# Kernel tuning notes

Measured on AMD Instinct MI355X. Metric: run time of the kernel, lower is better.

The kernel has to match this reference:

```python
import jax, jax.numpy as jnp
import numpy as np

DEGREE = 8
HIDDEN = 256
IN_DIM = 3
N_LAYERS = 8  # num_hidden_layers=8 -> 1 input + 6 middle + 1 output ChebyKAN layers


def cheby_layer(x, coeff):
    """x: [P, in], coeff: [in, out, degree+1] -> [P, out].
    Computes tanh(x), Chebyshev recurrence T_0..T_d, and contracts
    sum_d T_d(x)_i * coeff[i, o, d] without materializing the full basis.
    """
    x = jnp.tanh(x)
    t_prev = jnp.ones_like(x)          # T_0
    t_cur = x                          # T_1
    out = jnp.einsum('pi,io->po', t_prev, coeff[:, :, 0])
    out = out + jnp.einsum('pi,io->po', t_cur, coeff[:, :, 1])
    for d in range(2, coeff.shape[-1]):
        t_prev, t_cur = t_cur, 2.0 * x * t_cur - t_prev
        out = out + jnp.einsum('pi,io->po', t_cur, coeff[:, :, d])
    return out


def decode(pts, ws):
    h = pts
    for w in ws:
        h = cheby_layer(h, w)
    return h


def setup_inputs() -> dict:
    key = jax.random.key(0)
    k_nm, k_m, *k_ws = jax.random.split(key, 2 + N_LAYERS)
    B, N = 4, 16384
    inp = {
        'non_mnfld_pnts': jax.random.normal(k_nm, (B, N, IN_DIM), dtype=jnp.float32),
        'mnfld_pnts': jax.random.normal(k_m, (B, N, IN_DIM), dtype=jnp.float32),
    }
    dims = [IN_DIM] + [HIDDEN] * (N_LAYERS - 1) + [1]
    for i in range(N_LAYERS):
        fan_in, fan_out = dims[i], dims[i + 1]
        std = 1.0 / (fan_in * (DEGREE + 1))
        inp[f'w{i}'] = jax.random.normal(k_ws[i], (fan_in, fan_out, DEGREE + 1), dtype=jnp.float32) * std
    return inp


def reference(non_mnfld_pnts, mnfld_pnts, w0, w1, w2, w3, w4, w5, w6, w7):
    ws = [w0, w1, w2, w3, w4, w5, w6, w7]
    B = non_mnfld_pnts.shape[0]
    mnfld_pred = decode(mnfld_pnts.reshape(-1, IN_DIM), ws).reshape(B, -1)
    nonmnfld_pred = decode(non_mnfld_pnts.reshape(-1, IN_DIM), ws).reshape(B, -1)
    return (mnfld_pred, nonmnfld_pred)
```

## Files before the change

### kernel.cpp

```cpp
#include <hip/hip_runtime.h>

typedef _Float16 f16;
typedef __attribute__((ext_vector_type(4)))  _Float16 f16x4;
typedef __attribute__((ext_vector_type(8)))  _Float16 f16x8;
typedef __attribute__((ext_vector_type(16))) float    f32x16;

#define WT_L (8*256*256)

__device__ __forceinline__ float fexp2(float x) {
#if __has_builtin(__builtin_amdgcn_exp2f)
    return __builtin_amdgcn_exp2f(x);
#else
    return exp2f(x);
#endif
}

__device__ __forceinline__ float fast_tanh(float v) {
    float a = __builtin_fabsf(v);
    float e = fexp2(a * -2.8853900817779268f);
    float r = (1.0f - e) * __builtin_amdgcn_rcpf(1.0f + e);
    return __builtin_copysignf(r, v);
}

__global__ void prep_all(const float* __restrict__ w0, const float* __restrict__ w1,
                         const float* __restrict__ w2, const float* __restrict__ w3,
                         const float* __restrict__ w4, const float* __restrict__ w5,
                         const float* __restrict__ w6, const float* __restrict__ w7,
                         f16* __restrict__ wt, float* __restrict__ biasp,
                         float* __restrict__ w0t, float* __restrict__ w7p)
{
    __shared__ float red[256];
    const int bi = blockIdx.x, t = threadIdx.x;
    if (bi < 1536) {
        const int L = bi >> 8, o = bi & 255, i = t;
        const float* w;
        switch (L) { case 0: w = w1; break; case 1: w = w2; break; case 2: w = w3; break;
                     case 3: w = w4; break; case 4: w = w5; break; default: w = w6; }
        float v[9];
#pragma unroll
        for (int d = 0; d < 9; d++) v[d] = w[(i*256 + o)*9 + d];
        const int ck = i >> 4, k = i & 15;
        const int wv4 = o >> 6, nt = (o >> 5) & 1, l31 = o & 31;
        const int lane = (k >> 3)*32 + l31, e = k & 7;
        const int base = ck*4096 + wv4*1024 + nt*512 + lane*8 + e;
#pragma unroll
        for (int d = 1; d < 9; d++)
            wt[L*WT_L + (d-1)*16*4096 + base] = (f16)v[d];
        red[i] = v[0];
        __syncthreads();
#pragma unroll
        for (int s = 128; s > 0; s >>= 1) {
            if (i < s) red[i] += red[i + s];
            __syncthreads();
        }
        if (i == 0) biasp[L*256 + o] = red[0];
    } else if (bi < 1563) {
        int id = (bi - 1536)*256 + t;
        int i = id / 2304, rem = id % 2304;
        int o = rem / 9, d = rem % 9;
        w0t[(i*9 + d)*256 + o] = w0[id];
    } else {
        int id = (bi - 1563)*256 + t;
        int ch = id / 9, d = id % 9;
        w7p[ch*12 + d] = w7[id];
    }
}

__global__ void k0(const float* __restrict__ nonm, const float* __restrict__ mnf,
                   const float* __restrict__ w0t, f16* __restrict__ xg) {
    __shared__ __align__(16) f16 sh[64*256];
    const int t = threadIdx.x, b = blockIdx.x;
    const int pt = t & 63;
    const int oh = (t >> 6) * 64;
    const int pid = b*64 + pt;
    const float* src = (pid < 65536) ? mnf : nonm;
    const int sp = (pid < 65536) ? pid : pid - 65536;
    float c0 = src[sp*3 + 0];
    float c1 = src[sp*3 + 1];
    float c2 = src[sp*3 + 2];
    float xx[3] = {fast_tanh(c0), fast_tanh(c1), fast_tanh(c2)};
    float bas[27];
#pragma unroll
    for (int i = 0; i < 3; i++) {
        float t0 = 1.0f, t1 = xx[i];
        bas[i*9+0] = t0; bas[i*9+1] = t1;
        float x2 = xx[i] + xx[i];
#pragma unroll
        for (int d = 2; d < 9; d++) {
            float t2 = x2*t1 - t0;
            bas[i*9+d] = t2; t0 = t1; t1 = t2;
        }
    }
#pragma unroll 1
    for (int q = 0; q < 16; q++) {
        int o = oh + q*4;
        float4 a = {0.f, 0.f, 0.f, 0.f};
#pragma unroll
        for (int k = 0; k < 27; k++) {
            float4 wv = *(const float4*)(w0t + k*256 + o);
            a.x = fmaf(bas[k], wv.x, a.x);
            a.y = fmaf(bas[k], wv.y, a.y);
            a.z = fmaf(bas[k], wv.z, a.z);
            a.w = fmaf(bas[k], wv.w, a.w);
        }
        f16x4 hv = {(f16)fast_tanh(a.x), (f16)fast_tanh(a.y),
                    (f16)fast_tanh(a.z), (f16)fast_tanh(a.w)};
        int unit = (o >> 3) ^ (pt & 7);
        *(f16x4*)(sh + pt*256 + unit*8 + (o & 7)) = hv;
    }
    __syncthreads();
#pragma unroll
    for (int i = 0; i < 8; i++) {
        int idx = i*256 + t;
        int p2 = idx >> 5, cu = idx & 31;
        f16x8 v = *(const f16x8*)(sh + p2*256 + ((cu ^ (p2 & 7))*8));
        *(f16x8*)(xg + (size_t)b*16384 + (size_t)idx*8) = v;
    }
}

__global__ __launch_bounds__(256, 2)
void k_mid(const f16* __restrict__ wl, const float* __restrict__ biasL,
           f16* __restrict__ xg)
{
    __shared__ __align__(16) f16 xs[128*256];

    const int t    = threadIdx.x;
    const int b    = blockIdx.x;
    const int lane = t & 63;
    const int w    = t >> 6;
    const int l31  = lane & 31;
    const int half = lane >> 5;
    const int nb   = w * 64;
    const size_t tile_off = (size_t)b * 32768;

#pragma unroll
    for (int i = 0; i < 16; i++) {
        int idx = i*256 + t;
        int pt = idx >> 5, cu = idx & 31;
        f16x8 v = *(const f16x8*)(xg + tile_off + (size_t)idx*8);
        *(f16x8*)(xs + pt*256 + ((cu ^ (pt & 7))*8)) = v;
    }
    __syncthreads();

    f32x16 acc[4][2];
    const f16x8 ones = {(f16)1.f,(f16)1.f,(f16)1.f,(f16)1.f,(f16)1.f,(f16)1.f,(f16)1.f,(f16)1.f};

    const f16* wbase = wl + w*1024 + lane*8;
    float b0 = biasL[nb + l31];
    float b1 = biasL[nb + 32 + l31];
#pragma unroll
    for (int mt = 0; mt < 4; mt++)
#pragma unroll
        for (int r = 0; r < 16; r++) { acc[mt][0][r] = b0; acc[mt][1][r] = b1; }

    f16x8 xv[4], Bb[4][2];
#pragma unroll
    for (int mt = 0; mt < 4; mt++) {
        int m = mt*32 + l31;
        int unit = half ^ (m & 7);
        xv[mt] = *(const f16x8*)(xs + m*256 + unit*8);
    }
#pragma unroll
    for (int j = 0; j < 4; j++) {
        Bb[j][0] = *(const f16x8*)(wbase + j*16*4096);
        Bb[j][1] = *(const f16x8*)(wbase + j*16*4096 + 512);
    }

    f16x8 t1[4], t0v[4];
#pragma unroll 1
    for (int ck = 0; ck < 16; ck++) {
        const int ckn = (ck < 15) ? ck + 1 : 15;
#pragma unroll
        for (int mt = 0; mt < 4; mt++) {
            t1[mt]  = xv[mt];
            t0v[mt] = ones;
        }
#pragma unroll
        for (int j = 0; j < 8; j++) {
            const int ck2 = (j < 4) ? ck : ckn;
            const int j2  = (j < 4) ? (j + 4) : (j - 4);
            const int off = (j2*16 + ck2)*4096;
            f16x8 pb0 = *(const f16x8*)(wbase + off);
            f16x8 pb1 = *(const f16x8*)(wbase + off + 512);
#pragma unroll
            for (int mt = 0; mt < 4; mt++) {
                acc[mt][0] = __builtin_amdgcn_mfma_f32_32x32x16_f16(t1[mt], Bb[j&3][0], acc[mt][0], 0, 0, 0);
                acc[mt][1] = __builtin_amdgcn_mfma_f32_32x32x16_f16(t1[mt], Bb[j&3][1], acc[mt][1], 0, 0, 0);
            }
            if (j < 7) {
#pragma unroll
                for (int mt = 0; mt < 4; mt++) {
                    f16x8 tn = xv[mt]*(t1[mt] + t1[mt]) - t0v[mt];
                    t0v[mt] = t1[mt];
                    t1[mt]  = tn;
                }
            }
            if (j == 6) {
#pragma unroll
                for (int mt = 0; mt < 4; mt++) {
                    int m = mt*32 + l31;
                    int unit = (ckn*2 + half) ^ (m & 7);
                    xv[mt] = *(const f16x8*)(xs + m*256 + unit*8);
                }
            }
            Bb[j&3][0] = pb0;
            Bb[j&3][1] = pb1;
        }
    }
    __syncthreads();

#pragma unroll
    for (int mt = 0; mt < 4; mt++) {
#pragma unroll
        for (int nt = 0; nt < 2; nt++) {
            int ch = nb + nt*32 + l31;
            int cu = ch >> 3, ce = ch & 7;
#pragma unroll
            for (int r = 0; r < 16; r++) {
                int p = mt*32 + (r & 3) + 8*(r >> 2) + 4*half;
                int unit = cu ^ (p & 7);
                xs[p*256 + unit*8 + ce] = (f16)fast_tanh(acc[mt][nt][r]);
            }
        }
    }
    __syncthreads();

#pragma unroll
    for (int i = 0; i < 16; i++) {
        int idx = i*256 + t;
        int pt = idx >> 5, cu = idx & 31;
        f16x8 v = *(const f16x8*)(xs + pt*256 + ((cu ^ (pt & 7))*8));
        *(f16x8*)(xg + tile_off + (size_t)idx*8) = v;
    }
}

__global__ void k7(const f16* __restrict__ xg, const float* __restrict__ w7p,
                   float* __restrict__ out) {
    __shared__ __align__(16) f16 sh[128*256];
    const int t = threadIdx.x, b = blockIdx.x;
    const size_t tile_off = (size_t)b * 32768;
#pragma unroll
    for (int i = 0; i < 16; i++) {
        int idx = i*256 + t;
        int pt = idx >> 5, cu = idx & 31;
        f16x8 v = *(const f16x8*)(xg + tile_off + (size_t)idx*8);
        *(f16x8*)(sh + pt*256 + ((cu ^ (pt & 7))*8)) = v;
    }
    __syncthreads();

    const int pt = t & 127;
    const int seg = t >> 7;
    float s = 0.0f;
#pragma unroll 1
    for (int q = 0; q < 16; q++) {
        int u = seg*16 + q;
        int unit = u ^ (pt & 7);
        f16x8 xv = *(const f16x8*)(sh + pt*256 + unit*8);
#pragma unroll
        for (int e = 0; e < 8; e++) {
            int ch = u*8 + e;
            const float* wr = w7p + ch*12;
            float x = (float)xv[e];
            float4 wa = *(const float4*)(wr);
            float4 wb = *(const float4*)(wr + 4);
            float wc = wr[8];
            float x2 = x + x;
            float t0 = 1.0f, t1v = x;
            s = fmaf(wa.x, t0, s);
            s = fmaf(wa.y, t1v, s);
            float t2 = x2*t1v - t0;  s = fmaf(wa.z, t2, s);
            float t3 = x2*t2 - t1v;  s = fmaf(wa.w, t3, s);
            float t4 = x2*t3 - t2;   s = fmaf(wb.x, t4, s);
            float t5 = x2*t4 - t3;   s = fmaf(wb.y, t5, s);
            float t6 = x2*t5 - t4;   s = fmaf(wb.z, t6, s);
            float t7 = x2*t6 - t5;   s = fmaf(wb.w, t7, s);
            float t8 = x2*t7 - t6;   s = fmaf(wc,  t8, s);
        }
    }
    __syncthreads();
    float* red = (float*)sh;
    red[seg*128 + pt] = s;
    __syncthreads();
    if (t < 128) out[b*128 + t] = red[t] + red[128 + t];
}

extern "C" void kernel_launch(void* const* d_in, const int* in_sizes, int n_in,
                              void* d_out, int out_size, void* d_ws, size_t ws_size,
                              hipStream_t stream) {
    const float* nonm = (const float*)d_in[0];
    const float* mnf  = (const float*)d_in[1];

    char* ws = (char*)d_ws;
    f16*   wtp   = (f16*)ws;
    float* biasp = (float*)(ws + 6*WT_L*2);
    float* w0tp  = (float*)(ws + 6*WT_L*2 + 6144);
    float* w7pp  = (float*)(ws + 6*WT_L*2 + 6144 + 27648);
    f16*   xg    = (f16*)(ws + 6*WT_L*2 + 6144 + 27648 + 12288);

    prep_all<<<1572, 256, 0, stream>>>((const float*)d_in[2], (const float*)d_in[3],
                                       (const float*)d_in[4], (const float*)d_in[5],
                                       (const float*)d_in[6], (const float*)d_in[7],
                                       (const float*)d_in[8], (const float*)d_in[9],
                                       wtp, biasp, w0tp, w7pp);

    k0<<<2048, 256, 0, stream>>>(nonm, mnf, w0tp, xg);
    for (int L = 0; L < 6; L++)
        k_mid<<<1024, 256, 0, stream>>>(wtp + L*WT_L, biasp + L*256, xg);
    k7<<<1024, 256, 0, stream>>>(xg, w7pp, (float*)d_out);
}
```

Measured before the change: 1.071 ms.

## Fuse input layer and last layer into adjacent MFMA layer kernels

Folds the first Chebyshev layer (tanh, basis and 27-term FMA) into the first MFMA hidden-layer kernel, and the final scalar output layer into the last MFMA kernel, so two global activation round trips and two launches go away. The shared GEMM body is factored into a device function. It also precomputes 2x once per chunk and moves the next-chunk LDS load of x to the start of the chunk rather than inside the inner loop. In exchange the fused kernels carry more per-block work, and the layer-0 prologue now processes 128 points per block with two threads per point.

```diff
diff --git a/kernel.cpp b/kernel.cpp
--- a/kernel.cpp
+++ b/kernel.cpp
@@ -66,81 +66,16 @@
     }
 }
 
-__global__ void k0(const float* __restrict__ nonm, const float* __restrict__ mnf,
-                   const float* __restrict__ w0t, f16* __restrict__ xg) {
-    __shared__ __align__(16) f16 sh[64*256];
-    const int t = threadIdx.x, b = blockIdx.x;
-    const int pt = t & 63;
-    const int oh = (t >> 6) * 64;
-    const int pid = b*64 + pt;
-    const float* src = (pid < 65536) ? mnf : nonm;
-    const int sp = (pid < 65536) ? pid : pid - 65536;
-    float c0 = src[sp*3 + 0];
-    float c1 = src[sp*3 + 1];
-    float c2 = src[sp*3 + 2];
-    float xx[3] = {fast_tanh(c0), fast_tanh(c1), fast_tanh(c2)};
-    float bas[27];
-#pragma unroll
-    for (int i = 0; i < 3; i++) {
-        float t0 = 1.0f, t1 = xx[i];
-        bas[i*9+0] = t0; bas[i*9+1] = t1;
-        float x2 = xx[i] + xx[i];
-#pragma unroll
-        for (int d = 2; d < 9; d++) {
-            float t2 = x2*t1 - t0;
-            bas[i*9+d] = t2; t0 = t1; t1 = t2;
-        }
-    }
-#pragma unroll 1
-    for (int q = 0; q < 16; q++) {
-        int o = oh + q*4;
-        float4 a = {0.f, 0.f, 0.f, 0.f};
-#pragma unroll
-        for (int k = 0; k < 27; k++) {
-            float4 wv = *(const float4*)(w0t + k*256 + o);
-            a.x = fmaf(bas[k], wv.x, a.x);
-            a.y = fmaf(bas[k], wv.y, a.y);
-            a.z = fmaf(bas[k], wv.z, a.z);
-            a.w = fmaf(bas[k], wv.w, a.w);
-        }
-        f16x4 hv = {(f16)fast_tanh(a.x), (f16)fast_tanh(a.y),
-                    (f16)fast_tanh(a.z), (f16)fast_tanh(a.w)};
-        int unit = (o >> 3) ^ (pt & 7);
-        *(f16x4*)(sh + pt*256 + unit*8 + (o & 7)) = hv;
-    }
-    __syncthreads();
-#pragma unroll
-    for (int i = 0; i < 8; i++) {
-        int idx = i*256 + t;
-        int p2 = idx >> 5, cu = idx & 31;
-        f16x8 v = *(const f16x8*)(sh + p2*256 + ((cu ^ (p2 & 7))*8));
-        *(f16x8*)(xg + (size_t)b*16384 + (size_t)idx*8) = v;
-    }
-}
-
-__global__ __launch_bounds__(256, 2)
-void k_mid(const f16* __restrict__ wl, const float* __restrict__ biasL,
-           f16* __restrict__ xg)
-{
-    __shared__ __align__(16) f16 xs[128*256];
-
-    const int t    = threadIdx.x;
-    const int b    = blockIdx.x;
+__device__ __forceinline__ void gemm_layer(f16* __restrict__ xs,
+                                           const f16* __restrict__ wl,
+                                           const float* __restrict__ biasL,
+                                           int t)
+{
     const int lane = t & 63;
     const int w    = t >> 6;
     const int l31  = lane & 31;
     const int half = lane >> 5;
     const int nb   = w * 64;
-    const size_t tile_off = (size_t)b * 32768;
-
-#pragma unroll
-    for (int i = 0; i < 16; i++) {
-        int idx = i*256 + t;
-        int pt = idx >> 5, cu = idx & 31;
-        f16x8 v = *(const f16x8*)(xg + tile_off + (size_t)idx*8);
-        *(f16x8*)(xs + pt*256 + ((cu ^ (pt & 7))*8)) = v;
-    }
-    __syncthreads();
 
     f32x16 acc[4][2];
     const f16x8 ones = {(f16)1.f,(f16)1.f,(f16)1.f,(f16)1.f,(f16)1.f,(f16)1.f,(f16)1.f,(f16)1.f};
@@ -166,14 +101,21 @@
         Bb[j][1] = *(const f16x8*)(wbase + j*16*4096 + 512);
     }
 
-    f16x8 t1[4], t0v[4];
+    f16x8 x2[4], t1[4], t0v[4];
 #pragma unroll 1
     for (int ck = 0; ck < 16; ck++) {
         const int ckn = (ck < 15) ? ck + 1 : 15;
 #pragma unroll
         for (int mt = 0; mt < 4; mt++) {
             t1[mt]  = xv[mt];
+            x2[mt]  = xv[mt] + xv[mt];
             t0v[mt] = ones;
+        }
+#pragma unroll
+        for (int mt = 0; mt < 4; mt++) {
+            int m = mt*32 + l31;
+            int unit = (ckn*2 + half) ^ (m & 7);
+            xv[mt] = *(const f16x8*)(xs + m*256 + unit*8);
         }
 #pragma unroll
         for (int j = 0; j < 8; j++) {
@@ -190,17 +132,9 @@
             if (j < 7) {
 #pragma unroll
                 for (int mt = 0; mt < 4; mt++) {
-                    f16x8 tn = xv[mt]*(t1[mt] + t1[mt]) - t0v[mt];
+                    f16x8 tn = x2[mt]*t1[mt] - t0v[mt];
                     t0v[mt] = t1[mt];
                     t1[mt]  = tn;
-                }
-            }
-            if (j == 6) {
-#pragma unroll
-                for (int mt = 0; mt < 4; mt++) {
-                    int m = mt*32 + l31;
-                    int unit = (ckn*2 + half) ^ (m & 7);
-                    xv[mt] = *(const f16x8*)(xs + m*256 + unit*8);
                 }
             }
             Bb[j&3][0] = pb0;
@@ -224,7 +158,61 @@
         }
     }
     __syncthreads();
-
+}
+
+__global__ __launch_bounds__(256, 2)
+void kA(const float* __restrict__ nonm, const float* __restrict__ mnf,
+        const float* __restrict__ w0t, const f16* __restrict__ wt,
+        const float* __restrict__ biasL, f16* __restrict__ xg)
+{
+    __shared__ __align__(16) f16 xs[128*256];
+    const int t = threadIdx.x, b = blockIdx.x;
+
+    {
+        const int pt = t >> 1;
+        const int oh = (t & 1) * 128;
+        const int pid = b*128 + pt;
+        const float* src = (pid < 65536) ? mnf : nonm;
+        const int sp = (pid < 65536) ? pid : pid - 65536;
+        float c0 = src[sp*3 + 0];
+        float c1 = src[sp*3 + 1];
+        float c2 = src[sp*3 + 2];
+        float xx[3] = {fast_tanh(c0), fast_tanh(c1), fast_tanh(c2)};
+        float bas[27];
+#pragma unroll
+        for (int i = 0; i < 3; i++) {
+            float t0 = 1.0f, t1 = xx[i];
+            bas[i*9+0] = t0; bas[i*9+1] = t1;
+            float x2 = xx[i] + xx[i];
+#pragma unroll
+            for (int d = 2; d < 9; d++) {
+                float t2 = x2*t1 - t0;
+                bas[i*9+d] = t2; t0 = t1; t1 = t2;
+            }
+        }
+#pragma unroll 1
+        for (int q = 0; q < 32; q++) {
+            int o = oh + q*4;
+            float4 a = {0.f, 0.f, 0.f, 0.f};
+#pragma unroll
+            for (int k = 0; k < 27; k++) {
+                float4 wv = *(const float4*)(w0t + k*256 + o);
+                a.x = fmaf(bas[k], wv.x, a.x);
+                a.y = fmaf(bas[k], wv.y, a.y);
+                a.z = fmaf(bas[k], wv.z, a.z);
+                a.w = fmaf(bas[k], wv.w, a.w);
+            }
+            f16x4 hv = {(f16)fast_tanh(a.x), (f16)fast_tanh(a.y),
+                        (f16)fast_tanh(a.z), (f16)fast_tanh(a.w)};
+            int unit = (o >> 3) ^ (pt & 7);
+            *(f16x4*)(xs + pt*256 + unit*8 + (o & 7)) = hv;
+        }
+    }
+    __syncthreads();
+
+    gemm_layer(xs, wt, biasL, t);
+
+    const size_t tile_off = (size_t)b * 32768;
 #pragma unroll
     for (int i = 0; i < 16; i++) {
         int idx = i*256 + t;
@@ -234,54 +222,90 @@
     }
 }
 
-__global__ void k7(const f16* __restrict__ xg, const float* __restrict__ w7p,
-                   float* __restrict__ out) {
-    __shared__ __align__(16) f16 sh[128*256];
+__global__ __launch_bounds__(256, 2)
+void k_mid(const f16* __restrict__ wl, const float* __restrict__ biasL,
+           f16* __restrict__ xg)
+{
+    __shared__ __align__(16) f16 xs[128*256];
     const int t = threadIdx.x, b = blockIdx.x;
     const size_t tile_off = (size_t)b * 32768;
+
 #pragma unroll
     for (int i = 0; i < 16; i++) {
         int idx = i*256 + t;
         int pt = idx >> 5, cu = idx & 31;
         f16x8 v = *(const f16x8*)(xg + tile_off + (size_t)idx*8);
-        *(f16x8*)(sh + pt*256 + ((cu ^ (pt & 7))*8)) = v;
-    }
-    __syncthreads();
-
-    const int pt = t & 127;
-    const int seg = t >> 7;
-    float s = 0.0f;
+        *(f16x8*)(xs + pt*256 + ((cu ^ (pt & 7))*8)) = v;
+    }
+    __syncthreads();
+
+    gemm_layer(xs, wl, biasL, t);
+
+#pragma unroll
+    for (int i = 0; i < 16; i++) {
+        int idx = i*256 + t;
+        int pt = idx >> 5, cu = idx & 31;
+        f16x8 v = *(const f16x8*)(xs + pt*256 + ((cu ^ (pt & 7))*8));
+        *(f16x8*)(xg + tile_off + (size_t)idx*8) = v;
+    }
+}
+
+__global__ __launch_bounds__(256, 2)
+void kC(const f16* __restrict__ wt, const float* __restrict__ biasL,
+        const float* __restrict__ w7p, const f16* __restrict__ xg,
+        float* __restrict__ out)
+{
+    __shared__ __align__(16) f16 xs[128*256];
+    const int t = threadIdx.x, b = blockIdx.x;
+    const size_t tile_off = (size_t)b * 32768;
+
+#pragma unroll
+    for (int i = 0; i < 16; i++) {
+        int idx = i*256 + t;
+        int pt = idx >> 5, cu = idx & 31;
+        f16x8 v = *(const f16x8*)(xg + tile_off + (size_t)idx*8);
+        *(f16x8*)(xs + pt*256 + ((cu ^ (pt & 7))*8)) = v;
+    }
+    __syncthreads();
+
+    gemm_layer(xs, wt, biasL, t);
+
+    {
+        const int pt = t & 127;
+        const int seg = t >> 7;
+        float s = 0.0f;
 #pragma unroll 1
-    for (int q = 0; q < 16; q++) {
-        int u = seg*16 + q;
-        int unit = u ^ (pt & 7);
-        f16x8 xv = *(const f16x8*)(sh + pt*256 + unit*8);
-#pragma unroll
-        for (int e = 0; e < 8; e++) {
-            int ch = u*8 + e;
-            const float* wr = w7p + ch*12;
-            float x = (float)xv[e];
-            float4 wa = *(const float4*)(wr);
-            float4 wb = *(const float4*)(wr + 4);
-            float wc = wr[8];
-            float x2 = x + x;
-            float t0 = 1.0f, t1v = x;
-            s = fmaf(wa.x, t0, s);
-            s = fmaf(wa.y, t1v, s);
-            float t2 = x2*t1v - t0;  s = fmaf(wa.z, t2, s);
-            float t3 = x2*t2 - t1v;  s = fmaf(wa.w, t3, s);
-            float t4 = x2*t3 - t2;   s = fmaf(wb.x, t4, s);
-            float t5 = x2*t4 - t3;   s = fmaf(wb.y, t5, s);
-            float t6 = x2*t5 - t4;   s = fmaf(wb.z, t6, s);
-            float t7 = x2*t6 - t5;   s = fmaf(wb.w, t7, s);
-            float t8 = x2*t7 - t6;   s = fmaf(wc,  t8, s);
-        }
-    }
-    __syncthreads();
-    float* red = (float*)sh;
-    red[seg*128 + pt] = s;
-    __syncthreads();
-    if (t < 128) out[b*128 + t] = red[t] + red[128 + t];
+        for (int q = 0; q < 16; q++) {
+            int u = seg*16 + q;
+            int unit = u ^ (pt & 7);
+            f16x8 xv = *(const f16x8*)(xs + pt*256 + unit*8);
+#pragma unroll
+            for (int e = 0; e < 8; e++) {
+                int ch = u*8 + e;
+                const float* wr = w7p + ch*12;
+                float x = (float)xv[e];
+                float4 wa = *(const float4*)(wr);
+                float4 wb = *(const float4*)(wr + 4);
+                float wc = wr[8];
+                float x2 = x + x;
+                float t0 = 1.0f, t1v = x;
+                s = fmaf(wa.x, t0, s);
+                s = fmaf(wa.y, t1v, s);
+                float t2 = x2*t1v - t0;  s = fmaf(wa.z, t2, s);
+                float t3 = x2*t2 - t1v;  s = fmaf(wa.w, t3, s);
+                float t4 = x2*t3 - t2;   s = fmaf(wb.x, t4, s);
+                float t5 = x2*t4 - t3;   s = fmaf(wb.y, t5, s);
+                float t6 = x2*t5 - t4;   s = fmaf(wb.z, t6, s);
+                float t7 = x2*t6 - t5;   s = fmaf(wb.w, t7, s);
+                float t8 = x2*t7 - t6;   s = fmaf(wc,  t8, s);
+            }
+        }
+        __syncthreads();
+        float* red = (float*)xs;
+        red[seg*128 + pt] = s;
+        __syncthreads();
+        if (t < 128) out[b*128 + t] = red[t] + red[128 + t];
+    }
 }
 
 extern "C" void kernel_launch(void* const* d_in, const int* in_sizes, int n_in,
@@ -303,8 +327,8 @@
                                        (const float*)d_in[8], (const float*)d_in[9],
                                        wtp, biasp, w0tp, w7pp);
 
-    k0<<<2048, 256, 0, stream>>>(nonm, mnf, w0tp, xg);
-    for (int L = 0; L < 6; L++)
+    kA<<<1024, 256, 0, stream>>>(nonm, mnf, w0tp, wtp + 0*WT_L, biasp + 0*256, xg);
+    for (int L = 1; L < 5; L++)
         k_mid<<<1024, 256, 0, stream>>>(wtp + L*WT_L, biasp + L*256, xg);
-    k7<<<1024, 256, 0, stream>>>(xg, w7pp, (float*)d_out);
-}
+    kC<<<1024, 256, 0, stream>>>(wtp + 5*WT_L, biasp + 5*256, w7pp, xg, (float*)d_out);
+}
```

New measurement: 1.028 ms. 4.0% less time.
